# Kernel optimization log

Hardware: AMD Instinct MI355X
Metric: run time of the kernel (lower is better)

The kernel has to match this reference:

```python
import jax, jax.numpy as jnp
import numpy as np

N = 50000   # nodes
E = 800000  # edges
IN, HID, OUT = 128, 128, 64


def setup_inputs() -> dict:
    key = jax.random.key(0)
    ks = jax.random.split(key, 16)
    x = jax.random.normal(ks[0], (N, IN), dtype=jnp.float32)
    src = jax.random.randint(ks[1], (E,), 0, N, dtype=jnp.int32)
    dst = jax.random.randint(ks[2], (E,), 0, N, dtype=jnp.int32)
    s = 1.0 / np.sqrt(IN)
    W_self1 = jax.random.normal(ks[3], (IN, HID), dtype=jnp.float32) * s
    W_neigh1 = jax.random.normal(ks[4], (IN, HID), dtype=jnp.float32) * s
    b1 = jnp.zeros((HID,), dtype=jnp.float32)
    W_self2 = jax.random.normal(ks[5], (HID, HID), dtype=jnp.float32) * s
    W_neigh2 = jax.random.normal(ks[6], (HID, HID), dtype=jnp.float32) * s
    b2 = jnp.zeros((HID,), dtype=jnp.float32)
    W_self3 = jax.random.normal(ks[7], (HID, OUT), dtype=jnp.float32) * s
    W_neigh3 = jax.random.normal(ks[8], (HID, OUT), dtype=jnp.float32) * s
    b3 = jnp.zeros((OUT,), dtype=jnp.float32)
    # dropout(p=0.5) masks, pre-scaled by 1/(1-p)
    keep = 0.5
    mask1 = (jax.random.uniform(ks[9], (N, HID)) < keep).astype(jnp.float32) / keep
    mask2 = (jax.random.uniform(ks[10], (N, HID)) < keep).astype(jnp.float32) / keep
    return dict(x=x, src=src, dst=dst,
                W_self1=W_self1, W_neigh1=W_neigh1, b1=b1,
                W_self2=W_self2, W_neigh2=W_neigh2, b2=b2,
                W_self3=W_self3, W_neigh3=W_neigh3, b3=b3,
                mask1=mask1, mask2=mask2)


def _mean_agg(h, src, dst):
    # gather source features, segment-sum into destinations, divide by in-degree
    summed = jax.ops.segment_sum(h[src], dst, num_segments=N)  # [N, d]
    deg = jax.ops.segment_sum(jnp.ones((E,), dtype=h.dtype), dst, num_segments=N)
    return summed / jnp.maximum(deg, 1.0)[:, None]


def _sage_layer(h, src, dst, W_self, W_neigh, b):
    h_neigh = _mean_agg(h, src, dst)
    return h @ W_self + h_neigh @ W_neigh + b


def reference(x, src, dst, W_self1, W_neigh1, b1, W_self2, W_neigh2, b2,
              W_self3, W_neigh3, b3, mask1, mask2):
    h = _sage_layer(x, src, dst, W_self1, W_neigh1, b1)
    h = jax.nn.relu(h) * mask1
    h = _sage_layer(h, src, dst, W_self2, W_neigh2, b2)
    h = jax.nn.relu(h) * mask2
    h = _sage_layer(h, src, dst, W_self3, W_neigh3, b3)
    return h
```

## Files before the change

kernel.cpp:

```cpp
#include <hip/hip_runtime.h>
#include <hip/hip_bf16.h>

#define DIN  128
#define DHID 128
#define DOUT 64

#define EB   2048
#define CAPB 5120

typedef short short8 __attribute__((ext_vector_type(8)));
typedef float f32x4  __attribute__((ext_vector_type(4)));

__device__ __forceinline__ ushort f2bf(float f) {
    union { float f; uint u; } c; c.f = f;
    uint u = c.u;
    return (ushort)((u + 0x7fff + ((u >> 16) & 1)) >> 16);
}
__device__ __forceinline__ float bf2f(uint h16) {
    union { uint u; float f; } c; c.u = h16 << 16;
    return c.f;
}
__device__ __forceinline__ float sb8(uint u, int k) {
    return (float)((int)(u << (24 - 8 * k)) >> 24);
}

__device__ __forceinline__ void wprep_dev(const float* __restrict__ W,
                                          ushort* __restrict__ Wt, int OUT, int idx) {
    int nn = idx >> 7;
    int k  = idx & 127;
    Wt[idx] = f2bf(W[(size_t)k * OUT + nn]);
}

__global__ __launch_bounds__(256)
void megaprep(const int* __restrict__ src, const int* __restrict__ dst, int E, int fillB,
              int* __restrict__ bkt_cur, uint* __restrict__ pairs,
              const float* __restrict__ Ws1, const float* __restrict__ Wn1,
              const float* __restrict__ Ws2, const float* __restrict__ Wn2,
              const float* __restrict__ Ws3, const float* __restrict__ Wn3,
              ushort* __restrict__ Wst1, ushort* __restrict__ Wnt1,
              ushort* __restrict__ Wst2, ushort* __restrict__ Wnt2,
              ushort* __restrict__ Wst3, ushort* __restrict__ Wnt3) {
    __shared__ int c[256];
    __shared__ int startl[256];
    __shared__ int ofs[256];
    int b = blockIdx.x;
    const int t = threadIdx.x;
    if (b < fillB) {
        c[t] = 0;
        __syncthreads();
        const int base = b * EB;
        const int end = min(base + EB, E);
        if (end - base == EB) {
            int dl[8], sl[8];
#pragma unroll
            for (int r = 0; r < 8; ++r) {
                dl[r] = dst[base + t + r * 256];
                sl[r] = src[base + t + r * 256];
            }
#pragma unroll
            for (int r = 0; r < 8; ++r) atomicAdd(&c[dl[r] >> 8], 1);
            __syncthreads();
            int v = c[t];
            startl[t] = v ? (t * CAPB + atomicAdd(&bkt_cur[t], v)) : 0;
            ofs[t] = 0;
            __syncthreads();
#pragma unroll
            for (int r = 0; r < 8; ++r) {
                int d = dl[r];
                int bb = d >> 8;
                int p = startl[bb] + atomicAdd(&ofs[bb], 1);
                pairs[p] = ((uint)sl[r] << 8) | (uint)(d & 255);
            }
        } else {
            for (int i = base + t; i < end; i += 256)
                atomicAdd(&c[dst[i] >> 8], 1);
            __syncthreads();
            int v = c[t];
            startl[t] = v ? (t * CAPB + atomicAdd(&bkt_cur[t], v)) : 0;
            ofs[t] = 0;
            __syncthreads();
            for (int i = base + t; i < end; i += 256) {
                int d = dst[i];
                int bb = d >> 8;
                int p = startl[bb] + atomicAdd(&ofs[bb], 1);
                pairs[p] = ((uint)src[i] << 8) | (uint)(d & 255);
            }
        }
        return;
    }
    b -= fillB;
    if (b < 64)  { wprep_dev(Ws1, Wst1, 128, b * 256 + t); return; }
    b -= 64;
    if (b < 64)  { wprep_dev(Wn1, Wnt1, 128, b * 256 + t); return; }
    b -= 64;
    if (b < 64)  { wprep_dev(Ws2, Wst2, 128, b * 256 + t); return; }
    b -= 64;
    if (b < 64)  { wprep_dev(Wn2, Wnt2, 128, b * 256 + t); return; }
    b -= 64;
    if (b < 32)  { wprep_dev(Ws3, Wst3, 64, b * 256 + t); return; }
    b -= 32;
    wprep_dev(Wn3, Wnt3, 64, b * 256 + t);
}

__global__ __launch_bounds__(1024)
void csr_gemm1(const uint* __restrict__ pairs, const int* __restrict__ bkt_cur,
               int* __restrict__ row_ptr, int* __restrict__ deg,
               int* __restrict__ esrc, int N, int nbkt,
               const float* __restrict__ X,
               const ushort* __restrict__ Wst, const ushort* __restrict__ Wnt,
               ushort* __restrict__ S, signed char* __restrict__ Gq,
               float* __restrict__ Gsc) {
    __shared__ __align__(16) char smem[65536];
    const int tid = threadIdx.x;
    int b = blockIdx.x;

    if (b < nbkt) {
        constexpr int CAP = 6144;
        uint* pl  = (uint*)smem;
        int*  cnt = (int*)(smem + 24576);
        int*  rs  = (int*)(smem + 25600);
        int*  sc  = (int*)(smem + 26624);
        const int bkt = b;
        const int ebase = bkt * CAPB;
        const int ecnt  = min(bkt_cur[bkt], CAPB);
        if (tid < 256) cnt[tid] = 0;
        __syncthreads();
        const bool fits = (ecnt <= CAP);
        if (fits) {
            for (int i = tid; i < ecnt; i += 1024) {
                uint p = pairs[ebase + i];
                pl[i] = p;
                atomicAdd(&cnt[p & 255u], 1);
            }
        } else {
            for (int i = tid; i < ecnt; i += 1024)
                atomicAdd(&cnt[pairs[ebase + i] & 255u], 1);
        }
        __syncthreads();
        int own = 0;
        if (tid < 256) { own = cnt[tid]; sc[tid] = own; }
        __syncthreads();
        for (int o = 1; o < 256; o <<= 1) {
            int u = (tid < 256 && tid >= o) ? sc[tid - o] : 0;
            __syncthreads();
            if (tid < 256) sc[tid] += u;
            __syncthreads();
        }
        if (tid < 256) {
            rs[tid] = sc[tid] - own;
            const int node = bkt * 256 + tid;
            if (node < N) {
                row_ptr[node] = ebase + rs[tid];
                deg[node] = own;
            }
        }
        __syncthreads();
        if (fits) {
            for (int i = tid; i < ecnt; i += 1024) {
                uint p = pl[i];
                int pos = atomicAdd(&rs[p & 255u], 1);
                esrc[ebase + pos] = (int)(p >> 8);
            }
        } else {
            for (int i = tid; i < ecnt; i += 1024) {
                uint p = pairs[ebase + i];
                int pos = atomicAdd(&rs[p & 255u], 1);
                esrc[ebase + pos] = (int)(p >> 8);
            }
        }
        return;
    }

    b -= nbkt;
    constexpr int OUTW = 128;
    constexpr int NT = OUTW / 16;
    ushort* Wl = (ushort*)smem;

    {
        const uint4* s4 = (const uint4*)Wst;
        const uint4* n4 = (const uint4*)Wnt;
        uint4* ls = (uint4*)Wl;
        uint4* ln = (uint4*)(Wl + OUTW * 128);
#pragma unroll
        for (int j = tid; j < OUTW * 128 / 8; j += 1024) {
            ls[j] = s4[j];
            ln[j] = n4[j];
        }
    }

    const int vb   = tid >> 8;
    const int t2   = tid & 255;
    const int lane = t2 & 63;
    const int rg   = t2 >> 7;
    const int isG  = (t2 >> 6) & 1;
    const int m16  = lane & 15;
    const int kb   = lane >> 4;
    const int rbase = b * 256 + vb * 64 + rg * 32;
    const int n = N;

    short8 a[2][4];
#pragma unroll
    for (int mt = 0; mt < 2; ++mt) {
        int arow = rbase + mt * 16 + m16;
        if (arow >= n) arow = n - 1;
        const float* __restrict__ Ap = &X[(size_t)arow * 128 + kb * 8];
#pragma unroll
        for (int c = 0; c < 4; ++c) {
            float4 f0 = *(const float4*)(Ap + c * 32);
            float4 f1 = *(const float4*)(Ap + c * 32 + 4);
            short8 v;
            v[0] = (short)f2bf(f0.x); v[1] = (short)f2bf(f0.y);
            v[2] = (short)f2bf(f0.z); v[3] = (short)f2bf(f0.w);
            v[4] = (short)f2bf(f1.x); v[5] = (short)f2bf(f1.y);
            v[6] = (short)f2bf(f1.z); v[7] = (short)f2bf(f1.w);
            a[mt][c] = v;
        }
    }

    __syncthreads();

    f32x4 acc[2][NT];
#pragma unroll
    for (int mt = 0; mt < 2; ++mt)
#pragma unroll
        for (int t = 0; t < NT; ++t) acc[mt][t] = (f32x4)(0.f);

    const ushort* __restrict__ Wp = &Wl[isG * OUTW * 128];
#pragma unroll
    for (int t = 0; t < NT; ++t) {
#pragma unroll
        for (int c = 0; c < 4; ++c) {
            short8 bb = *(const short8*)&Wp[(t * 16 + m16) * 128 + c * 32 + kb * 8];
            acc[0][t] = __builtin_amdgcn_mfma_f32_16x16x32_bf16(a[0][c], bb, acc[0][t], 0, 0, 0);
            acc[1][t] = __builtin_amdgcn_mfma_f32_16x16x32_bf16(a[1][c], bb, acc[1][t], 0, 0, 0);
        }
    }

#pragma unroll
    for (int mt = 0; mt < 2; ++mt) {
        const int rb = rbase + mt * 16;
        if (!isG) {
#pragma unroll
            for (int r = 0; r < 4; ++r) {
                int row = rb + kb * 4 + r;
                if (row >= n) continue;
#pragma unroll
                for (int t = 0; t < NT; ++t)
                    S[(size_t)row * OUTW + t * 16 + m16] = f2bf(acc[mt][t][r]);
            }
        } else {
#pragma unroll
            for (int r = 0; r < 4; ++r) {
                float mx = 0.f;
#pragma unroll
                for (int t = 0; t < NT; ++t) mx = fmaxf(mx, fabsf(acc[mt][t][r]));
                mx = fmaxf(mx, __shfl_xor(mx, 1));
                mx = fmaxf(mx, __shfl_xor(mx, 2));
                mx = fmaxf(mx, __shfl_xor(mx, 4));
                mx = fmaxf(mx, __shfl_xor(mx, 8));
                int row = rb + kb * 4 + r;
                if (row >= n) continue;
                float inv = (mx > 0.f) ? 127.f / mx : 0.f;
                if (m16 == 0) Gsc[row] = mx * (1.f / 127.f);
#pragma unroll
                for (int t = 0; t < NT; ++t) {
                    int q = (int)rintf(acc[mt][t][r] * inv);
                    q = max(-127, min(127, q));
                    Gq[(size_t)row * OUTW + t * 16 + m16] = (signed char)q;
                }
            }
        }
    }
}

template<int OUTW>
__global__ __launch_bounds__(256)
void sage_gemm(const ushort* __restrict__ Hb,
               const ushort* __restrict__ Wst,
               const ushort* __restrict__ Wnt,
               ushort* __restrict__ S,
               signed char* __restrict__ Gq,
               float* __restrict__ Gsc,
               int n) {
    constexpr int NT = OUTW / 16;
    __shared__ ushort Wl[2][OUTW * 128];

    const int tid  = threadIdx.x;
    const int lane = tid & 63;
    const int wave = tid >> 6;
    const int rg   = wave >> 1;
    const int isG  = wave & 1;
    const int m16  = lane & 15;
    const int kb   = lane >> 4;
    const int rbase = blockIdx.x * 64 + rg * 32;

    {
        const uint4* s4 = (const uint4*)Wst;
        const uint4* n4 = (const uint4*)Wnt;
        uint4* ls = (uint4*)&Wl[0][0];
        uint4* ln = (uint4*)&Wl[1][0];
#pragma unroll
        for (int j = tid; j < OUTW * 128 / 8; j += 256) {
            ls[j] = s4[j];
            ln[j] = n4[j];
        }
    }

    short8 a[2][4];
#pragma unroll
    for (int mt = 0; mt < 2; ++mt) {
        int arow = rbase + mt * 16 + m16;
        if (arow >= n) arow = n - 1;
        const ushort* __restrict__ Ap = &Hb[(size_t)arow * 128 + kb * 8];
#pragma unroll
        for (int c = 0; c < 4; ++c)
            a[mt][c] = *(const short8*)(Ap + c * 32);
    }

    __syncthreads();

    f32x4 acc[2][NT];
#pragma unroll
    for (int mt = 0; mt < 2; ++mt)
#pragma unroll
        for (int t = 0; t < NT; ++t) acc[mt][t] = (f32x4)(0.f);

    const ushort* __restrict__ Wp = &Wl[isG][0];
#pragma unroll
    for (int t = 0; t < NT; ++t) {
#pragma unroll
        for (int c = 0; c < 4; ++c) {
            short8 b = *(const short8*)&Wp[(t * 16 + m16) * 128 + c * 32 + kb * 8];
            acc[0][t] = __builtin_amdgcn_mfma_f32_16x16x32_bf16(a[0][c], b, acc[0][t], 0, 0, 0);
            acc[1][t] = __builtin_amdgcn_mfma_f32_16x16x32_bf16(a[1][c], b, acc[1][t], 0, 0, 0);
        }
    }

#pragma unroll
    for (int mt = 0; mt < 2; ++mt) {
        const int rb = rbase + mt * 16;
        if (!isG) {
#pragma unroll
            for (int r = 0; r < 4; ++r) {
                int row = rb + kb * 4 + r;
                if (row >= n) continue;
#pragma unroll
                for (int t = 0; t < NT; ++t)
                    S[(size_t)row * OUTW + t * 16 + m16] = f2bf(acc[mt][t][r]);
            }
        } else {
#pragma unroll
            for (int r = 0; r < 4; ++r) {
                float mx = 0.f;
#pragma unroll
                for (int t = 0; t < NT; ++t) mx = fmaxf(mx, fabsf(acc[mt][t][r]));
                mx = fmaxf(mx, __shfl_xor(mx, 1));
                mx = fmaxf(mx, __shfl_xor(mx, 2));
                mx = fmaxf(mx, __shfl_xor(mx, 4));
                mx = fmaxf(mx, __shfl_xor(mx, 8));
                int row = rb + kb * 4 + r;
                if (row >= n) continue;
                float inv = (mx > 0.f) ? 127.f / mx : 0.f;
                if (m16 == 0) Gsc[row] = mx * (1.f / 127.f);
#pragma unroll
                for (int t = 0; t < NT; ++t) {
                    int q = (int)rintf(acc[mt][t][r] * inv);
                    q = max(-127, min(127, q));
                    Gq[(size_t)row * OUTW + t * 16 + m16] = (signed char)q;
                }
            }
        }
    }
}

__device__ __forceinline__ void acc8(float* af, uint2 v, float sc) {
    af[0] += sc * sb8(v.x, 0); af[1] += sc * sb8(v.x, 1);
    af[2] += sc * sb8(v.x, 2); af[3] += sc * sb8(v.x, 3);
    af[4] += sc * sb8(v.y, 0); af[5] += sc * sb8(v.y, 1);
    af[6] += sc * sb8(v.y, 2); af[7] += sc * sb8(v.y, 3);
}
__device__ __forceinline__ void acc16(float* af, uint4 v, float sc) {
    af[0]  += sc * sb8(v.x, 0); af[1]  += sc * sb8(v.x, 1);
    af[2]  += sc * sb8(v.x, 2); af[3]  += sc * sb8(v.x, 3);
    af[4]  += sc * sb8(v.y, 0); af[5]  += sc * sb8(v.y, 1);
    af[6]  += sc * sb8(v.y, 2); af[7]  += sc * sb8(v.y, 3);
    af[8]  += sc * sb8(v.z, 0); af[9]  += sc * sb8(v.z, 1);
    af[10] += sc * sb8(v.z, 2); af[11] += sc * sb8(v.z, 3);
    af[12] += sc * sb8(v.w, 0); af[13] += sc * sb8(v.w, 1);
    af[14] += sc * sb8(v.w, 2); af[15] += sc * sb8(v.w, 3);
}

#define WCAP 320

#define LOADT16(V, C, j_)                                           \
    _Pragma("unroll")                                               \
    for (int k = 0; k < 4; ++k) {                                   \
        int p_ = i0 + (j_) * 4 + k;                                 \
        bool ok_ = p_ < e_;                                         \
        uint2 pr_ = iw[ok_ ? p_ : i0];                              \
        V[k] = *(const uint4*)&gp[(size_t)pr_.x * 128];             \
        C[k] = ok_ ? __uint_as_float(pr_.y) : 0.f;                  \
    }
#define LOADT8(V, C, j_)                                            \
    _Pragma("unroll")                                               \
    for (int k = 0; k < 4; ++k) {                                   \
        int p_ = i0 + (j_) * 4 + k;                                 \
        bool ok_ = p_ < e_;                                         \
        uint2 pr_ = iw[ok_ ? p_ : i0];                              \
        V[k] = *(const uint2*)&gp[(size_t)pr_.x * 64];              \
        C[k] = ok_ ? __uint_as_float(pr_.y) : 0.f;                  \
    }
#define CONST16(V, C)                                               \
    _Pragma("unroll") for (int k = 0; k < 4; ++k) acc16(af, V[k], C[k]);
#define CONST8(V, C)                                                \
    _Pragma("unroll") for (int k = 0; k < 4; ++k) acc8(af, V[k], C[k]);

template<bool FINAL>
__global__ __launch_bounds__(128)
void sage_gather(const signed char* __restrict__ Gq, const float* __restrict__ Gsc,
                 const ushort* __restrict__ S, const float* __restrict__ bias,
                 const float* __restrict__ mask,
                 const int* __restrict__ row_ptr, const int* __restrict__ deg,
                 const int* __restrict__ esrc,
                 void* __restrict__ outv, int n) {
    __shared__ uint2 is_s[2][WCAP];

    const int tid  = threadIdx.x;
    const int wave = tid >> 6;
    const int lane = tid & 63;
    const int g    = lane >> 3;
    const int l8   = lane & 7;
    const int wbase = blockIdx.x * 16 + wave * 8;
    if (wbase >= n) return;

    const int node = wbase + g;
    int d = 0, rp = 0;
    if (node < n) { d = deg[node]; rp = row_ptr[node]; }

    const int last   = min(wbase + 7, n - 1);
    const int span_s = row_ptr[wbase];
    const int span_e = row_ptr[last] + deg[last];
    const int len    = span_e - span_s;
    uint2* __restrict__ iw = is_s[wave];
    const bool staged = (len <= WCAP);
    if (staged) {
        int sA[5];
#pragma unroll
        for (int r = 0; r < 5; ++r) {
            int i = lane + r * 64;
            sA[r] = (i < len) ? esrc[span_s + i] : 0;
        }
#pragma unroll
        for (int r = 0; r < 5; ++r) {
            int i = lane + r * 64;
            if (i < len)
                iw[i] = make_uint2((uint)sA[r], __float_as_uint(Gsc[sA[r]]));
        }
    }

    if (node >= n) return;
    const float inv = 1.f / fmaxf((float)d, 1.f);

    if (!FINAL) {
        float af[16];
#pragma unroll
        for (int q = 0; q < 16; ++q) af[q] = 0.f;
        const signed char* __restrict__ gp = Gq + l8 * 16;
        const int col0 = l8 * 16;

        uint4 sa = *(const uint4*)&S[(size_t)node * 128 + col0];
        uint4 sb = *(const uint4*)&S[(size_t)node * 128 + col0 + 8];
        float bv[16], mv[16];
#pragma unroll
        for (int q = 0; q < 4; ++q) {
            *(float4*)&bv[q * 4] = *(const float4*)&bias[col0 + q * 4];
            *(float4*)&mv[q * 4] = *(const float4*)&mask[(size_t)node * 128 + col0 + q * 4];
        }

        if (staged) {
            const int i0 = rp - span_s;
            const int e_ = i0 + d;
            const int nb = (d + 3) >> 2;
            uint4 vA[4], vB[4], vC[4]; float cA[4], cB[4], cC[4];
            if (nb > 0) {
                LOADT16(vA, cA, 0);
                if (nb > 1) { LOADT16(vB, cB, 1); }
                if (nb > 2) { LOADT16(vC, cC, 2); }
                int b = 0;
                while (true) {
                    CONST16(vA, cA);
                    if (b + 3 < nb) { LOADT16(vA, cA, b + 3); }
                    ++b; if (b >= nb) break;
                    CONST16(vB, cB);
                    if (b + 3 < nb) { LOADT16(vB, cB, b + 3); }
                    ++b; if (b >= nb) break;
                    CONST16(vC, cC);
                    if (b + 3 < nb) { LOADT16(vC, cC, b + 3); }
                    ++b; if (b >= nb) break;
                }
            }
        } else {
            int i = rp, e = i + d;
            for (; i < e; ++i) {
                int ns = esrc[i];
                acc16(af, *(const uint4*)&gp[(size_t)ns * 128], Gsc[ns]);
            }
        }
        uint sv[8] = {sa.x, sa.y, sa.z, sa.w, sb.x, sb.y, sb.z, sb.w};
        uint pk[8];
#pragma unroll
        for (int q = 0; q < 8; ++q) {
            float z0 = bf2f(sv[q] & 0xffffu) + af[2 * q]     * inv + bv[2 * q];
            float z1 = bf2f(sv[q] >> 16)     + af[2 * q + 1] * inv + bv[2 * q + 1];
            z0 = fmaxf(z0, 0.f) * mv[2 * q];
            z1 = fmaxf(z1, 0.f) * mv[2 * q + 1];
            pk[q] = (uint)f2bf(z0) | ((uint)f2bf(z1) << 16);
        }
        ushort* op = (ushort*)outv + (size_t)node * 128 + col0;
        uint4 o0, o1;
        o0.x = pk[0]; o0.y = pk[1]; o0.z = pk[2]; o0.w = pk[3];
        o1.x = pk[4]; o1.y = pk[5]; o1.z = pk[6]; o1.w = pk[7];
        *(uint4*)op = o0;
        *(uint4*)(op + 8) = o1;
    } else {
        float af[8];
#pragma unroll
        for (int q = 0; q < 8; ++q) af[q] = 0.f;
        const signed char* __restrict__ gp = Gq + l8 * 8;
        const int col0 = l8 * 8;

        uint4 sv4 = *(const uint4*)&S[(size_t)node * 64 + col0];
        float bv[8];
        *(float4*)&bv[0] = *(const float4*)&bias[col0];
        *(float4*)&bv[4] = *(const float4*)&bias[col0 + 4];

        if (staged) {
            const int i0 = rp - span_s;
            const int e_ = i0 + d;
            const int nb = (d + 3) >> 2;
            uint2 vA[4], vB[4], vC[4]; float cA[4], cB[4], cC[4];
            if (nb > 0) {
                LOADT8(vA, cA, 0);
                if (nb > 1) { LOADT8(vB, cB, 1); }
                if (nb > 2) { LOADT8(vC, cC, 2); }
                int b = 0;
                while (true) {
                    CONST8(vA, cA);
                    if (b + 3 < nb) { LOADT8(vA, cA, b + 3); }
                    ++b; if (b >= nb) break;
                    CONST8(vB, cB);
                    if (b + 3 < nb) { LOADT8(vB, cB, b + 3); }
                    ++b; if (b >= nb) break;
                    CONST8(vC, cC);
                    if (b + 3 < nb) { LOADT8(vC, cC, b + 3); }
                    ++b; if (b >= nb) break;
                }
            }
        } else {
            int i = rp, e = i + d;
            for (; i < e; ++i) {
                int ns = esrc[i];
                acc8(af, *(const uint2*)&gp[(size_t)ns * 64], Gsc[ns]);
            }
        }
        uint sv[4] = {sv4.x, sv4.y, sv4.z, sv4.w};
        float z[8];
#pragma unroll
        for (int q = 0; q < 4; ++q) {
            z[2 * q]     = bf2f(sv[q] & 0xffffu) + af[2 * q]     * inv + bv[2 * q];
            z[2 * q + 1] = bf2f(sv[q] >> 16)     + af[2 * q + 1] * inv + bv[2 * q + 1];
        }
        float* op = (float*)outv + (size_t)node * 64 + col0;
        float4 o0, o1;
        o0.x = z[0]; o0.y = z[1]; o0.z = z[2]; o0.w = z[3];
        o1.x = z[4]; o1.y = z[5]; o1.z = z[6]; o1.w = z[7];
        *(float4*)&op[0] = o0;
        *(float4*)&op[4] = o1;
    }
}

extern "C" void kernel_launch(void* const* d_in, const int* in_sizes, int n_in,
                              void* d_out, int out_size, void* d_ws, size_t ws_size,
                              hipStream_t stream) {
    const float* x   = (const float*)d_in[0];
    const int*   src = (const int*)d_in[1];
    const int*   dst = (const int*)d_in[2];
    const float* Ws1 = (const float*)d_in[3];
    const float* Wn1 = (const float*)d_in[4];
    const float* b1  = (const float*)d_in[5];
    const float* Ws2 = (const float*)d_in[6];
    const float* Wn2 = (const float*)d_in[7];
    const float* b2  = (const float*)d_in[8];
    const float* Ws3 = (const float*)d_in[9];
    const float* Wn3 = (const float*)d_in[10];
    const float* b3  = (const float*)d_in[11];
    const float* mask1 = (const float*)d_in[12];
    const float* mask2 = (const float*)d_in[13];
    float* out = (float*)d_out;

    const int N = in_sizes[0] / DIN;
    const int E = in_sizes[1];
    const int nbkt = (N + 255) >> 8;

    char* ws = (char*)d_ws;
    int* bkt_cur  = (int*)ws;
    int* row_ptr  = bkt_cur + 256;
    int* deg      = row_ptr + N;
    int* esrc     = deg + N;
    size_t off = ((size_t)(256 + 2 * N + nbkt * CAPB) * sizeof(int) + 255) & ~(size_t)255;
    uint* pairs  = (uint*)(ws + off);    off += (size_t)nbkt * CAPB * 4;
    ushort* h1b  = (ushort*)(ws + off);  off += (size_t)N * 128 * 2;
    ushort* h2b  = (ushort*)(ws + off);  off += (size_t)N * 128 * 2;
    ushort* S    = (ushort*)(ws + off);  off += (size_t)N * 128 * 2;
    signed char* Gq = (signed char*)(ws + off); off += (size_t)N * 128;
    float* Gsc   = (float*)(ws + off);   off += (size_t)N * 4;
    ushort* Wst1 = (ushort*)(ws + off);  off += 128 * 128 * 2;
    ushort* Wnt1 = (ushort*)(ws + off);  off += 128 * 128 * 2;
    ushort* Wst2 = (ushort*)(ws + off);  off += 128 * 128 * 2;
    ushort* Wnt2 = (ushort*)(ws + off);  off += 128 * 128 * 2;
    ushort* Wst3 = (ushort*)(ws + off);  off += 64 * 128 * 2;
    ushort* Wnt3 = (ushort*)(ws + off);  off += 64 * 128 * 2;

    const int fillB = (E + EB - 1) / EB;

    hipMemsetAsync(bkt_cur, 0, 256 * sizeof(int), stream);
    megaprep<<<fillB + 4 * 64 + 2 * 32, 256, 0, stream>>>(
        src, dst, E, fillB, bkt_cur, pairs,
        Ws1, Wn1, Ws2, Wn2, Ws3, Wn3,
        Wst1, Wnt1, Wst2, Wnt2, Wst3, Wnt3);

    const int g256 = (N + 255) / 256;
    csr_gemm1<<<nbkt + g256, 1024, 0, stream>>>(
        pairs, bkt_cur, row_ptr, deg, esrc, N, nbkt,
        x, Wst1, Wnt1, S, Gq, Gsc);

    const int gemmB = (N + 63) / 64;
    const int gathB = (N + 15) / 16;

    sage_gather<false><<<gathB, 128, 0, stream>>>(Gq, Gsc, S, b1, mask1, row_ptr, deg, esrc, h1b, N);
    sage_gemm<128><<<gemmB, 256, 0, stream>>>(h1b, Wst2, Wnt2, S, Gq, Gsc, N);
    sage_gather<false><<<gathB, 128, 0, stream>>>(Gq, Gsc, S, b2, mask2, row_ptr, deg, esrc, h2b, N);
    sage_gemm<64><<<gemmB, 256, 0, stream>>>(h2b, Wst3, Wnt3, S, Gq, Gsc, N);
    sage_gather<true><<<gathB, 128, 0, stream>>>(Gq, Gsc, S, b3, nullptr, row_ptr, deg, esrc, out, N);
}
```

Measured before the change: 269.2 us.

## Fuse neighbor gather with next-layer dual GEMM into one kernel

Merges each hidden layer's mean-aggregation/ReLU/dropout gather with the following self/neighbor GEMM, so the activated bf16 features stay in shared memory instead of round-tripping through global memory. Separate S/Gq/Gsc buffers per layer are allocated so a kernel never overwrites the buffers it reads. This drops two kernel launches and the h1/h2 write-plus-read traffic. In exchange, the GEMM reads weights straight from global or cache rather than from LDS, and each block carries more state, which may lower occupancy of the gather phase.

```diff
diff --git a/kernel.cpp b/kernel.cpp
--- a/kernel.cpp
+++ b/kernel.cpp
@@ -273,106 +273,6 @@
     }
 }
 
-template<int OUTW>
-__global__ __launch_bounds__(256)
-void sage_gemm(const ushort* __restrict__ Hb,
-               const ushort* __restrict__ Wst,
-               const ushort* __restrict__ Wnt,
-               ushort* __restrict__ S,
-               signed char* __restrict__ Gq,
-               float* __restrict__ Gsc,
-               int n) {
-    constexpr int NT = OUTW / 16;
-    __shared__ ushort Wl[2][OUTW * 128];
-
-    const int tid  = threadIdx.x;
-    const int lane = tid & 63;
-    const int wave = tid >> 6;
-    const int rg   = wave >> 1;
-    const int isG  = wave & 1;
-    const int m16  = lane & 15;
-    const int kb   = lane >> 4;
-    const int rbase = blockIdx.x * 64 + rg * 32;
-
-    {
-        const uint4* s4 = (const uint4*)Wst;
-        const uint4* n4 = (const uint4*)Wnt;
-        uint4* ls = (uint4*)&Wl[0][0];
-        uint4* ln = (uint4*)&Wl[1][0];
-#pragma unroll
-        for (int j = tid; j < OUTW * 128 / 8; j += 256) {
-            ls[j] = s4[j];
-            ln[j] = n4[j];
-        }
-    }
-
-    short8 a[2][4];
-#pragma unroll
-    for (int mt = 0; mt < 2; ++mt) {
-        int arow = rbase + mt * 16 + m16;
-        if (arow >= n) arow = n - 1;
-        const ushort* __restrict__ Ap = &Hb[(size_t)arow * 128 + kb * 8];
-#pragma unroll
-        for (int c = 0; c < 4; ++c)
-            a[mt][c] = *(const short8*)(Ap + c * 32);
-    }
-
-    __syncthreads();
-
-    f32x4 acc[2][NT];
-#pragma unroll
-    for (int mt = 0; mt < 2; ++mt)
-#pragma unroll
-        for (int t = 0; t < NT; ++t) acc[mt][t] = (f32x4)(0.f);
-
-    const ushort* __restrict__ Wp = &Wl[isG][0];
-#pragma unroll
-    for (int t = 0; t < NT; ++t) {
-#pragma unroll
-        for (int c = 0; c < 4; ++c) {
-            short8 b = *(const short8*)&Wp[(t * 16 + m16) * 128 + c * 32 + kb * 8];
-            acc[0][t] = __builtin_amdgcn_mfma_f32_16x16x32_bf16(a[0][c], b, acc[0][t], 0, 0, 0);
-            acc[1][t] = __builtin_amdgcn_mfma_f32_16x16x32_bf16(a[1][c], b, acc[1][t], 0, 0, 0);
-        }
-    }
-
-#pragma unroll
-    for (int mt = 0; mt < 2; ++mt) {
-        const int rb = rbase + mt * 16;
-        if (!isG) {
-#pragma unroll
-            for (int r = 0; r < 4; ++r) {
-                int row = rb + kb * 4 + r;
-                if (row >= n) continue;
-#pragma unroll
-                for (int t = 0; t < NT; ++t)
-                    S[(size_t)row * OUTW + t * 16 + m16] = f2bf(acc[mt][t][r]);
-            }
-        } else {
-#pragma unroll
-            for (int r = 0; r < 4; ++r) {
-                float mx = 0.f;
-#pragma unroll
-                for (int t = 0; t < NT; ++t) mx = fmaxf(mx, fabsf(acc[mt][t][r]));
-                mx = fmaxf(mx, __shfl_xor(mx, 1));
-                mx = fmaxf(mx, __shfl_xor(mx, 2));
-                mx = fmaxf(mx, __shfl_xor(mx, 4));
-                mx = fmaxf(mx, __shfl_xor(mx, 8));
-                int row = rb + kb * 4 + r;
-                if (row >= n) continue;
-                float inv = (mx > 0.f) ? 127.f / mx : 0.f;
-                if (m16 == 0) Gsc[row] = mx * (1.f / 127.f);
-#pragma unroll
-                for (int t = 0; t < NT; ++t) {
-                    int q = (int)rintf(acc[mt][t][r] * inv);
-                    q = max(-127, min(127, q));
-                    Gq[(size_t)row * OUTW + t * 16 + m16] = (signed char)q;
-                }
-            }
-        }
-    }
-}
-
 __device__ __forceinline__ void acc8(float* af, uint2 v, float sc) {
     af[0] += sc * sb8(v.x, 0); af[1] += sc * sb8(v.x, 1);
     af[2] += sc * sb8(v.x, 2); af[3] += sc * sb8(v.x, 3);
@@ -415,14 +315,200 @@
 #define CONST8(V, C)                                                \
     _Pragma("unroll") for (int k = 0; k < 4; ++k) acc8(af, V[k], C[k]);
 
-template<bool FINAL>
+template<int OUTW_NEXT>
+__global__ __launch_bounds__(256)
+void sage_fused(const signed char* __restrict__ Gq, const float* __restrict__ Gsc,
+                const ushort* __restrict__ S, const float* __restrict__ bias,
+                const float* __restrict__ mask,
+                const int* __restrict__ row_ptr, const int* __restrict__ deg,
+                const int* __restrict__ esrc,
+                const ushort* __restrict__ Wst, const ushort* __restrict__ Wnt,
+                ushort* __restrict__ S2, signed char* __restrict__ Gq2,
+                float* __restrict__ Gsc2, int n) {
+    constexpr int NTW = OUTW_NEXT / 32;
+    constexpr int HC  = OUTW_NEXT / 2;
+    __shared__ uint2  is_s[4][WCAP];
+    __shared__ ushort hl[32][136];
+    __shared__ float  gmax[2][32];
+
+    const int tid  = threadIdx.x;
+    const int wave = tid >> 6;
+    const int lane = tid & 63;
+    const int g    = lane >> 3;
+    const int l8   = lane & 7;
+    const int nbase = blockIdx.x * 32;
+    if (nbase >= n) return;
+    const int wbase = nbase + wave * 8;
+    const int node  = wbase + g;
+
+    if (wbase < n) {
+        int d = 0, rp = 0;
+        if (node < n) { d = deg[node]; rp = row_ptr[node]; }
+        const int last   = min(wbase + 7, n - 1);
+        const int span_s = row_ptr[wbase];
+        const int span_e = row_ptr[last] + deg[last];
+        const int len    = span_e - span_s;
+        uint2* __restrict__ iw = is_s[wave];
+        const bool staged = (len <= WCAP);
+        if (staged) {
+            int sA[5];
+#pragma unroll
+            for (int r = 0; r < 5; ++r) {
+                int i = lane + r * 64;
+                sA[r] = (i < len) ? esrc[span_s + i] : 0;
+            }
+#pragma unroll
+            for (int r = 0; r < 5; ++r) {
+                int i = lane + r * 64;
+                if (i < len)
+                    iw[i] = make_uint2((uint)sA[r], __float_as_uint(Gsc[sA[r]]));
+            }
+        }
+        if (node < n) {
+            const float inv = 1.f / fmaxf((float)d, 1.f);
+            float af[16];
+#pragma unroll
+            for (int q = 0; q < 16; ++q) af[q] = 0.f;
+            const signed char* __restrict__ gp = Gq + l8 * 16;
+            const int col0 = l8 * 16;
+            uint4 sa = *(const uint4*)&S[(size_t)node * 128 + col0];
+            uint4 sb = *(const uint4*)&S[(size_t)node * 128 + col0 + 8];
+            float bv[16], mv[16];
+#pragma unroll
+            for (int q = 0; q < 4; ++q) {
+                *(float4*)&bv[q * 4] = *(const float4*)&bias[col0 + q * 4];
+                *(float4*)&mv[q * 4] = *(const float4*)&mask[(size_t)node * 128 + col0 + q * 4];
+            }
+            if (staged) {
+                const int i0 = rp - span_s;
+                const int e_ = i0 + d;
+                const int nb = (d + 3) >> 2;
+                uint4 vA[4], vB[4], vC[4]; float cA[4], cB[4], cC[4];
+                if (nb > 0) {
+                    LOADT16(vA, cA, 0);
+                    if (nb > 1) { LOADT16(vB, cB, 1); }
+                    if (nb > 2) { LOADT16(vC, cC, 2); }
+                    int b = 0;
+                    while (true) {
+                        CONST16(vA, cA);
+                        if (b + 3 < nb) { LOADT16(vA, cA, b + 3); }
+                        ++b; if (b >= nb) break;
+                        CONST16(vB, cB);
+                        if (b + 3 < nb) { LOADT16(vB, cB, b + 3); }
+                        ++b; if (b >= nb) break;
+                        CONST16(vC, cC);
+                        if (b + 3 < nb) { LOADT16(vC, cC, b + 3); }
+                        ++b; if (b >= nb) break;
+                    }
+                }
+            } else {
+                int i = rp, e = i + d;
+                for (; i < e; ++i) {
+                    int ns = esrc[i];
+                    acc16(af, *(const uint4*)&gp[(size_t)ns * 128], Gsc[ns]);
+                }
+            }
+            uint sv[8] = {sa.x, sa.y, sa.z, sa.w, sb.x, sb.y, sb.z, sb.w};
+            uint* hp = (uint*)&hl[wave * 8 + g][col0];
+#pragma unroll
+            for (int q = 0; q < 8; ++q) {
+                float z0 = bf2f(sv[q] & 0xffffu) + af[2 * q]     * inv + bv[2 * q];
+                float z1 = bf2f(sv[q] >> 16)     + af[2 * q + 1] * inv + bv[2 * q + 1];
+                z0 = fmaxf(z0, 0.f) * mv[2 * q];
+                z1 = fmaxf(z1, 0.f) * mv[2 * q + 1];
+                hp[q] = (uint)f2bf(z0) | ((uint)f2bf(z1) << 16);
+            }
+        }
+    }
+    __syncthreads();
+
+    const int matsel = wave >> 1;
+    const int half   = wave & 1;
+    const int m16 = lane & 15;
+    const int kb  = lane >> 4;
+    const ushort* __restrict__ Wp = (matsel ? Wnt : Wst) + (size_t)(half * HC) * 128;
+
+    short8 a[2][4];
+#pragma unroll
+    for (int mt = 0; mt < 2; ++mt)
+#pragma unroll
+        for (int c = 0; c < 4; ++c)
+            a[mt][c] = *(const short8*)&hl[mt * 16 + m16][c * 32 + kb * 8];
+
+    f32x4 acc[2][NTW];
+#pragma unroll
+    for (int mt = 0; mt < 2; ++mt)
+#pragma unroll
+        for (int t = 0; t < NTW; ++t) acc[mt][t] = (f32x4)(0.f);
+
+#pragma unroll
+    for (int t = 0; t < NTW; ++t) {
+#pragma unroll
+        for (int c = 0; c < 4; ++c) {
+            short8 bb = *(const short8*)&Wp[(t * 16 + m16) * 128 + c * 32 + kb * 8];
+            acc[0][t] = __builtin_amdgcn_mfma_f32_16x16x32_bf16(a[0][c], bb, acc[0][t], 0, 0, 0);
+            acc[1][t] = __builtin_amdgcn_mfma_f32_16x16x32_bf16(a[1][c], bb, acc[1][t], 0, 0, 0);
+        }
+    }
+
+    if (matsel == 1) {
+#pragma unroll
+        for (int mt = 0; mt < 2; ++mt) {
+#pragma unroll
+            for (int r = 0; r < 4; ++r) {
+                float mx = 0.f;
+#pragma unroll
+                for (int t = 0; t < NTW; ++t) mx = fmaxf(mx, fabsf(acc[mt][t][r]));
+                mx = fmaxf(mx, __shfl_xor(mx, 1));
+                mx = fmaxf(mx, __shfl_xor(mx, 2));
+                mx = fmaxf(mx, __shfl_xor(mx, 4));
+                mx = fmaxf(mx, __shfl_xor(mx, 8));
+                if (m16 == 0) gmax[half][mt * 16 + kb * 4 + r] = mx;
+            }
+        }
+    }
+    __syncthreads();
+
+    if (matsel == 0) {
+#pragma unroll
+        for (int mt = 0; mt < 2; ++mt) {
+#pragma unroll
+            for (int r = 0; r < 4; ++r) {
+                int row = nbase + mt * 16 + kb * 4 + r;
+                if (row >= n) continue;
+#pragma unroll
+                for (int t = 0; t < NTW; ++t)
+                    S2[(size_t)row * OUTW_NEXT + half * HC + t * 16 + m16] = f2bf(acc[mt][t][r]);
+            }
+        }
+    } else {
+#pragma unroll
+        for (int mt = 0; mt < 2; ++mt) {
+#pragma unroll
+            for (int r = 0; r < 4; ++r) {
+                int lrow = mt * 16 + kb * 4 + r;
+                int row = nbase + lrow;
+                if (row >= n) continue;
+                float mx = fmaxf(gmax[0][lrow], gmax[1][lrow]);
+                float inv = (mx > 0.f) ? 127.f / mx : 0.f;
+                if (half == 0 && m16 == 0) Gsc2[row] = mx * (1.f / 127.f);
+#pragma unroll
+                for (int t = 0; t < NTW; ++t) {
+                    int q = (int)rintf(acc[mt][t][r] * inv);
+                    q = max(-127, min(127, q));
+                    Gq2[(size_t)row * OUTW_NEXT + half * HC + t * 16 + m16] = (signed char)q;
+                }
+            }
+        }
+    }
+}
+
 __global__ __launch_bounds__(128)
-void sage_gather(const signed char* __restrict__ Gq, const float* __restrict__ Gsc,
-                 const ushort* __restrict__ S, const float* __restrict__ bias,
-                 const float* __restrict__ mask,
-                 const int* __restrict__ row_ptr, const int* __restrict__ deg,
-                 const int* __restrict__ esrc,
-                 void* __restrict__ outv, int n) {
+void sage_gather_final(const signed char* __restrict__ Gq, const float* __restrict__ Gsc,
+                       const ushort* __restrict__ S, const float* __restrict__ bias,
+                       const int* __restrict__ row_ptr, const int* __restrict__ deg,
+                       const int* __restrict__ esrc,
+                       float* __restrict__ outv, int n) {
     __shared__ uint2 is_s[2][WCAP];
 
     const int tid  = threadIdx.x;
@@ -461,122 +547,59 @@
     if (node >= n) return;
     const float inv = 1.f / fmaxf((float)d, 1.f);
 
-    if (!FINAL) {
-        float af[16];
-#pragma unroll
-        for (int q = 0; q < 16; ++q) af[q] = 0.f;
-        const signed char* __restrict__ gp = Gq + l8 * 16;
-        const int col0 = l8 * 16;
-
-        uint4 sa = *(const uint4*)&S[(size_t)node * 128 + col0];
-        uint4 sb = *(const uint4*)&S[(size_t)node * 128 + col0 + 8];
-        float bv[16], mv[16];
-#pragma unroll
-        for (int q = 0; q < 4; ++q) {
-            *(float4*)&bv[q * 4] = *(const float4*)&bias[col0 + q * 4];
-            *(float4*)&mv[q * 4] = *(const float4*)&mask[(size_t)node * 128 + col0 + q * 4];
-        }
-
-        if (staged) {
-            const int i0 = rp - span_s;
-            const int e_ = i0 + d;
-            const int nb = (d + 3) >> 2;
-            uint4 vA[4], vB[4], vC[4]; float cA[4], cB[4], cC[4];
-            if (nb > 0) {
-                LOADT16(vA, cA, 0);
-                if (nb > 1) { LOADT16(vB, cB, 1); }
-                if (nb > 2) { LOADT16(vC, cC, 2); }
-                int b = 0;
-                while (true) {
-                    CONST16(vA, cA);
-                    if (b + 3 < nb) { LOADT16(vA, cA, b + 3); }
-                    ++b; if (b >= nb) break;
-                    CONST16(vB, cB);
-                    if (b + 3 < nb) { LOADT16(vB, cB, b + 3); }
-                    ++b; if (b >= nb) break;
-                    CONST16(vC, cC);
-                    if (b + 3 < nb) { LOADT16(vC, cC, b + 3); }
-                    ++b; if (b >= nb) break;
-                }
-            }
-        } else {
-            int i = rp, e = i + d;
-            for (; i < e; ++i) {
-                int ns = esrc[i];
-                acc16(af, *(const uint4*)&gp[(size_t)ns * 128], Gsc[ns]);
-            }
-        }
-        uint sv[8] = {sa.x, sa.y, sa.z, sa.w, sb.x, sb.y, sb.z, sb.w};
-        uint pk[8];
-#pragma unroll
-        for (int q = 0; q < 8; ++q) {
-            float z0 = bf2f(sv[q] & 0xffffu) + af[2 * q]     * inv + bv[2 * q];
-            float z1 = bf2f(sv[q] >> 16)     + af[2 * q + 1] * inv + bv[2 * q + 1];
-            z0 = fmaxf(z0, 0.f) * mv[2 * q];
-            z1 = fmaxf(z1, 0.f) * mv[2 * q + 1];
-            pk[q] = (uint)f2bf(z0) | ((uint)f2bf(z1) << 16);
-        }
-        ushort* op = (ushort*)outv + (size_t)node * 128 + col0;
-        uint4 o0, o1;
-        o0.x = pk[0]; o0.y = pk[1]; o0.z = pk[2]; o0.w = pk[3];
-        o1.x = pk[4]; o1.y = pk[5]; o1.z = pk[6]; o1.w = pk[7];
-        *(uint4*)op = o0;
-        *(uint4*)(op + 8) = o1;
+    float af[8];
+#pragma unroll
+    for (int q = 0; q < 8; ++q) af[q] = 0.f;
+    const signed char* __restrict__ gp = Gq + l8 * 8;
+    const int col0 = l8 * 8;
+
+    uint4 sv4 = *(const uint4*)&S[(size_t)node * 64 + col0];
+    float bv[8];
+    *(float4*)&bv[0] = *(const float4*)&bias[col0];
+    *(float4*)&bv[4] = *(const float4*)&bias[col0 + 4];
+
+    if (staged) {
+        const int i0 = rp - span_s;
+        const int e_ = i0 + d;
+        const int nb = (d + 3) >> 2;
+        uint2 vA[4], vB[4], vC[4]; float cA[4], cB[4], cC[4];
+        if (nb > 0) {
+            LOADT8(vA, cA, 0);
+            if (nb > 1) { LOADT8(vB, cB, 1); }
+            if (nb > 2) { LOADT8(vC, cC, 2); }
+            int b = 0;
+            while (true) {
+                CONST8(vA, cA);
+                if (b + 3 < nb) { LOADT8(vA, cA, b + 3); }
+                ++b; if (b >= nb) break;
+                CONST8(vB, cB);
+                if (b + 3 < nb) { LOADT8(vB, cB, b + 3); }
+                ++b; if (b >= nb) break;
+                CONST8(vC, cC);
+                if (b + 3 < nb) { LOADT8(vC, cC, b + 3); }
+                ++b; if (b >= nb) break;
+            }
+        }
     } else {
-        float af[8];
-#pragma unroll
-        for (int q = 0; q < 8; ++q) af[q] = 0.f;
-        const signed char* __restrict__ gp = Gq + l8 * 8;
-        const int col0 = l8 * 8;
-
-        uint4 sv4 = *(const uint4*)&S[(size_t)node * 64 + col0];
-        float bv[8];
-        *(float4*)&bv[0] = *(const float4*)&bias[col0];
-        *(float4*)&bv[4] = *(const float4*)&bias[col0 + 4];
-
-        if (staged) {
-            const int i0 = rp - span_s;
-            const int e_ = i0 + d;
-            const int nb = (d + 3) >> 2;
-            uint2 vA[4], vB[4], vC[4]; float cA[4], cB[4], cC[4];
-            if (nb > 0) {
-                LOADT8(vA, cA, 0);
-                if (nb > 1) { LOADT8(vB, cB, 1); }
-                if (nb > 2) { LOADT8(vC, cC, 2); }
-                int b = 0;
-                while (true) {
-                    CONST8(vA, cA);
-                    if (b + 3 < nb) { LOADT8(vA, cA, b + 3); }
-                    ++b; if (b >= nb) break;
-                    CONST8(vB, cB);
-                    if (b + 3 < nb) { LOADT8(vB, cB, b + 3); }
-                    ++b; if (b >= nb) break;
-                    CONST8(vC, cC);
-                    if (b + 3 < nb) { LOADT8(vC, cC, b + 3); }
-                    ++b; if (b >= nb) break;
-                }
-            }
-        } else {
-            int i = rp, e = i + d;
-            for (; i < e; ++i) {
-                int ns = esrc[i];
-                acc8(af, *(const uint2*)&gp[(size_t)ns * 64], Gsc[ns]);
-            }
-        }
-        uint sv[4] = {sv4.x, sv4.y, sv4.z, sv4.w};
-        float z[8];
-#pragma unroll
-        for (int q = 0; q < 4; ++q) {
-            z[2 * q]     = bf2f(sv[q] & 0xffffu) + af[2 * q]     * inv + bv[2 * q];
-            z[2 * q + 1] = bf2f(sv[q] >> 16)     + af[2 * q + 1] * inv + bv[2 * q + 1];
-        }
-        float* op = (float*)outv + (size_t)node * 64 + col0;
-        float4 o0, o1;
-        o0.x = z[0]; o0.y = z[1]; o0.z = z[2]; o0.w = z[3];
-        o1.x = z[4]; o1.y = z[5]; o1.z = z[6]; o1.w = z[7];
-        *(float4*)&op[0] = o0;
-        *(float4*)&op[4] = o1;
-    }
+        int i = rp, e = i + d;
+        for (; i < e; ++i) {
+            int ns = esrc[i];
+            acc8(af, *(const uint2*)&gp[(size_t)ns * 64], Gsc[ns]);
+        }
+    }
+    uint sv[4] = {sv4.x, sv4.y, sv4.z, sv4.w};
+    float z[8];
+#pragma unroll
+    for (int q = 0; q < 4; ++q) {
+        z[2 * q]     = bf2f(sv[q] & 0xffffu) + af[2 * q]     * inv + bv[2 * q];
+        z[2 * q + 1] = bf2f(sv[q] >> 16)     + af[2 * q + 1] * inv + bv[2 * q + 1];
+    }
+    float* op = outv + (size_t)node * 64 + col0;
+    float4 o0, o1;
+    o0.x = z[0]; o0.y = z[1]; o0.z = z[2]; o0.w = z[3];
+    o1.x = z[4]; o1.y = z[5]; o1.z = z[6]; o1.w = z[7];
+    *(float4*)&op[0] = o0;
+    *(float4*)&op[4] = o1;
 }
 
 extern "C" void kernel_launch(void* const* d_in, const int* in_sizes, int n_in,
@@ -608,18 +631,24 @@
     int* deg      = row_ptr + N;
     int* esrc     = deg + N;
     size_t off = ((size_t)(256 + 2 * N + nbkt * CAPB) * sizeof(int) + 255) & ~(size_t)255;
-    uint* pairs  = (uint*)(ws + off);    off += (size_t)nbkt * CAPB * 4;
-    ushort* h1b  = (ushort*)(ws + off);  off += (size_t)N * 128 * 2;
-    ushort* h2b  = (ushort*)(ws + off);  off += (size_t)N * 128 * 2;
-    ushort* S    = (ushort*)(ws + off);  off += (size_t)N * 128 * 2;
-    signed char* Gq = (signed char*)(ws + off); off += (size_t)N * 128;
-    float* Gsc   = (float*)(ws + off);   off += (size_t)N * 4;
-    ushort* Wst1 = (ushort*)(ws + off);  off += 128 * 128 * 2;
-    ushort* Wnt1 = (ushort*)(ws + off);  off += 128 * 128 * 2;
-    ushort* Wst2 = (ushort*)(ws + off);  off += 128 * 128 * 2;
-    ushort* Wnt2 = (ushort*)(ws + off);  off += 128 * 128 * 2;
-    ushort* Wst3 = (ushort*)(ws + off);  off += 64 * 128 * 2;
-    ushort* Wnt3 = (ushort*)(ws + off);  off += 64 * 128 * 2;
+#define ALLOC(ptr, type, bytes) type* ptr = (type*)(ws + off); off = (off + (bytes) + 255) & ~(size_t)255
+    ALLOC(pairs, uint,        (size_t)nbkt * CAPB * 4);
+    ALLOC(S_a,   ushort,      (size_t)N * 128 * 2);
+    ALLOC(S_b,   ushort,      (size_t)N * 128 * 2);
+    ALLOC(S_c,   ushort,      (size_t)N * 64 * 2);
+    ALLOC(Gq_a,  signed char, (size_t)N * 128);
+    ALLOC(Gq_b,  signed char, (size_t)N * 128);
+    ALLOC(Gq_c,  signed char, (size_t)N * 64);
+    ALLOC(Gsc_a, float,       (size_t)N * 4);
+    ALLOC(Gsc_b, float,       (size_t)N * 4);
+    ALLOC(Gsc_c, float,       (size_t)N * 4);
+    ALLOC(Wst1,  ushort,      128 * 128 * 2);
+    ALLOC(Wnt1,  ushort,      128 * 128 * 2);
+    ALLOC(Wst2,  ushort,      128 * 128 * 2);
+    ALLOC(Wnt2,  ushort,      128 * 128 * 2);
+    ALLOC(Wst3,  ushort,      64 * 128 * 2);
+    ALLOC(Wnt3,  ushort,      64 * 128 * 2);
+#undef ALLOC
 
     const int fillB = (E + EB - 1) / EB;
 
@@ -632,14 +661,17 @@
     const int g256 = (N + 255) / 256;
     csr_gemm1<<<nbkt + g256, 1024, 0, stream>>>(
         pairs, bkt_cur, row_ptr, deg, esrc, N, nbkt,
-        x, Wst1, Wnt1, S, Gq, Gsc);
-
-    const int gemmB = (N + 63) / 64;
-    const int gathB = (N + 15) / 16;
-
-    sage_gather<false><<<gathB, 128, 0, stream>>>(Gq, Gsc, S, b1, mask1, row_ptr, deg, esrc, h1b, N);
-    sage_gemm<128><<<gemmB, 256, 0, stream>>>(h1b, Wst2, Wnt2, S, Gq, Gsc, N);
-    sage_gather<false><<<gathB, 128, 0, stream>>>(Gq, Gsc, S, b2, mask2, row_ptr, deg, esrc, h2b, N);
-    sage_gemm<64><<<gemmB, 256, 0, stream>>>(h2b, Wst3, Wnt3, S, Gq, Gsc, N);
-    sage_gather<true><<<gathB, 128, 0, stream>>>(Gq, Gsc, S, b3, nullptr, row_ptr, deg, esrc, out, N);
-}
+        x, Wst1, Wnt1, S_a, Gq_a, Gsc_a);
+
+    const int fusedB = (N + 31) / 32;
+    const int gathB  = (N + 15) / 16;
+
+    sage_fused<128><<<fusedB, 256, 0, stream>>>(
+        Gq_a, Gsc_a, S_a, b1, mask1, row_ptr, deg, esrc,
+        Wst2, Wnt2, S_b, Gq_b, Gsc_b, N);
+    sage_fused<64><<<fusedB, 256, 0, stream>>>(
+        Gq_b, Gsc_b, S_b, b2, mask2, row_ptr, deg, esrc,
+        Wst3, Wnt3, S_c, Gq_c, Gsc_c, N);
+    sage_gather_final<<<gathB, 128, 0, stream>>>(
+        Gq_c, Gsc_c, S_c, b3, row_ptr, deg, esrc, out, N);
+}
```

New measurement: 271.2 us. Within noise of the previous version (+0.7%).
